# Performance work log

Measured on AMD Instinct MI355X. Metric: run time of the kernel, lower is better.

Reference implementation:

```python
import jax, jax.numpy as jnp
import numpy as np

B, S, D, H = 2, 2048, 1024, 16
Dh = D // H
EPS = 1e-6


def _layernorm(x, alpha, beta):
    # torch.std is unbiased (ddof=1); module divides by (std + eps)
    m = jnp.mean(x, axis=-1, keepdims=True)
    var = jnp.sum((x - m) ** 2, axis=-1, keepdims=True) / (x.shape[-1] - 1)
    return alpha * (x - m) / (jnp.sqrt(var) + EPS) + beta


def setup_inputs() -> dict:
    key = jax.random.key(0)
    ks = jax.random.split(key, 12)
    sc = 0.02
    return {
        "x": jax.random.normal(ks[0], (B, S, D), jnp.float32),
        "src_mask": jnp.ones((B, 1, S), jnp.int32),
        # per-head q/k/v projections stacked over heads: [H, D, Dh]
        "Wq": jax.random.normal(ks[1], (H, D, Dh), jnp.float32) * sc,
        "bq": jnp.zeros((H, Dh), jnp.float32),
        "Wk": jax.random.normal(ks[2], (H, D, Dh), jnp.float32) * sc,
        "bk": jnp.zeros((H, Dh), jnp.float32),
        "Wv": jax.random.normal(ks[3], (H, D, Dh), jnp.float32) * sc,
        "bv": jnp.zeros((H, Dh), jnp.float32),
        # FFN: D -> 4D -> D
        "W1": jax.random.normal(ks[4], (D, 4 * D), jnp.float32) * sc,
        "b1": jnp.zeros((4 * D,), jnp.float32),
        "W2": jax.random.normal(ks[5], (4 * D, D), jnp.float32) * sc,
        "b2": jnp.zeros((D,), jnp.float32),
        # two LayerNorms (residual connections)
        "alpha1": jnp.ones((D,), jnp.float32),
        "beta1": jnp.zeros((D,), jnp.float32),
        "alpha2": jnp.ones((D,), jnp.float32),
        "beta2": jnp.zeros((D,), jnp.float32),
    }


def _encoder_block(x, src_mask, Wq, bq, Wk, bk, Wv, bv, W1, b1, W2, b2,
                   alpha1, beta1, alpha2, beta2):
    # --- multi-head self-attention (all heads vectorized) ---
    q = jnp.einsum('bsd,hde->bhse', x, Wq) + bq[None, :, None, :]
    k = jnp.einsum('bsd,hde->bhse', x, Wk) + bk[None, :, None, :]
    v = jnp.einsum('bsd,hde->bhse', x, Wv) + bv[None, :, None, :]
    wei = jnp.einsum('bhse,bhte->bhst', q, k) * (Dh ** -0.5)  # [B,H,S,S]
    wei = jnp.where(src_mask[:, None, :, :] == 0, -jnp.inf, wei)
    wei = jax.nn.softmax(wei, axis=-1)
    attn = jnp.einsum('bhst,bhte->bhse', wei, v)  # [B,H,S,Dh]
    attn = attn.transpose(0, 2, 1, 3).reshape(x.shape[0], x.shape[1], D)
    # NOTE: original module never applies its output projection (self.pro unused)
    # residual 1: x + norm(sublayer(x))
    x = x + _layernorm(attn, alpha1, beta1)
    # --- feed-forward ---
    h = jax.nn.relu(x @ W1 + b1)
    ffn = h @ W2 + b2
    x = x + _layernorm(ffn, alpha2, beta2)
    return x


def reference(x, src_mask, Wq, bq, Wk, bk, Wv, bv, W1, b1, W2, b2,
              alpha1, beta1, alpha2, beta2):
    return _encoder_block(x, src_mask, Wq, bq, Wk, bk, Wv, bv,
                          W1, b1, W2, b2, alpha1, beta1, alpha2, beta2)
```

## Files before the change

kernel.cpp:

```cpp
#include <hip/hip_runtime.h>


#define DEV __device__ __forceinline__

typedef unsigned short u16;
typedef unsigned int u32;
typedef __attribute__((ext_vector_type(8))) short bfrag;
typedef __attribute__((ext_vector_type(8))) __bf16 bf16x8;
typedef __attribute__((ext_vector_type(2))) __bf16 bf16x2_t;
typedef __attribute__((ext_vector_type(4))) unsigned int u32x4;
typedef __attribute__((ext_vector_type(4))) float facc;
typedef __attribute__((ext_vector_type(16))) float facc16;

DEV float bf2f(u16 u) {
  unsigned int x = ((unsigned int)u) << 16;
  return __builtin_bit_cast(float, x);
}
DEV u16 f2bf(float f) {
  unsigned int x = __builtin_bit_cast(unsigned int, f);
  x += 0x7fffu + ((x >> 16) & 1u);
  return (u16)(x >> 16);
}

DEV void gl2lds16(const u16* g, u16* l) {
  auto gp = (const __attribute__((address_space(1))) unsigned int*)(g);
  auto lp = (__attribute__((address_space(3))) unsigned int*)(l);
  __builtin_amdgcn_global_load_lds(gp, lp, 16, 0, 0);
}

DEV facc mfma16(bfrag a, bfrag b, facc c) {
  return __builtin_amdgcn_mfma_f32_16x16x32_bf16(
      __builtin_bit_cast(bf16x8, a), __builtin_bit_cast(bf16x8, b), c, 0, 0, 0);
}

DEV facc16 mfma32(bfrag a, bfrag b, facc16 c) {
  return __builtin_amdgcn_mfma_f32_32x32x16_bf16(
      __builtin_bit_cast(bf16x8, a), __builtin_bit_cast(bf16x8, b), c, 0, 0, 0);
}

DEV u32 pk2(float a, float b) {
  bf16x2_t v;
  v[0] = (__bf16)a;
  v[1] = (__bf16)b;
  return __builtin_bit_cast(u32, v);
}

DEV void pswap(u32& a, u32& b) {
  asm volatile("v_permlane32_swap_b32 %0, %1" : "+v"(a), "+v"(b));
}

__global__ __launch_bounds__(256) void prep_kernel(
    const float* __restrict__ Wq, const float* __restrict__ Wk,
    const float* __restrict__ Wv, u16* __restrict__ WqkvT,
    const float* __restrict__ W1, u16* __restrict__ W1T,
    const float* __restrict__ W2, u16* __restrict__ W2T,
    const float* __restrict__ x, u16* __restrict__ xb) {
  __shared__ float tile[32][33];
  const int job = blockIdx.x;
  const int tr = threadIdx.x >> 5, tc = threadIdx.x & 31;

  if (job >= 11264) {
    const int i = (job - 11264) * 1024 + threadIdx.x * 4;
    const float4 v = *(const float4*)(x + i);
    ushort4 o;
    o.x = f2bf(v.x); o.y = f2bf(v.y); o.z = f2bf(v.z); o.w = f2bf(v.w);
    *(ushort4*)(xb + i) = o;
    return;
  }

  const float* in;
  u16* out;
  int C, R, c0, r0;
  if (job < 3072) {
    const int z = job >> 6, rem = job & 63;
    const int which = z >> 4, h = z & 15;
    in = ((which == 0) ? Wq : (which == 1) ? Wk : Wv) + (size_t)h * 1024 * 64;
    out = WqkvT + ((size_t)which * 1024 + h * 64) * 1024;
    C = 64; R = 1024;
    c0 = (rem & 1) * 32; r0 = (rem >> 1) * 32;
  } else if (job < 7168) {
    const int rem = job - 3072;
    in = W1; out = W1T; C = 4096; R = 1024;
    c0 = (rem & 127) * 32; r0 = (rem >> 7) * 32;
  } else {
    const int rem = job - 7168;
    in = W2; out = W2T; C = 1024; R = 4096;
    c0 = (rem & 31) * 32; r0 = (rem >> 5) * 32;
  }
#pragma unroll
  for (int k = 0; k < 4; k++)
    tile[tr + 8 * k][tc] = in[(size_t)(r0 + tr + 8 * k) * C + c0 + tc];
  __syncthreads();
#pragma unroll
  for (int k = 0; k < 4; k++)
    out[(size_t)(c0 + tr + 8 * k) * R + r0 + tc] = f2bf(tile[tc][tr + 8 * k]);
}

template <int MODE>
__global__ __launch_bounds__(512, 2) void gemm256(
    const u16* __restrict__ A, int lda, const u16* __restrict__ Bt, int ldb,
    int M, int N, int K,
    const float* __restrict__ bias0, const float* __restrict__ bias1,
    const float* __restrict__ bias2,
    void* __restrict__ out0, void* __restrict__ out1, void* __restrict__ out2) {
  __shared__ __align__(16) u16 As[2][256 * 64];
  __shared__ __align__(16) u16 Bs[2][256 * 64];
  const int tid = threadIdx.x;
  const int lane = tid & 63;
  const int wave = tid >> 6;
  const int laneM = lane & 15, quad = lane >> 4;
  const int kx = laneM & 7;
  const int m0 = blockIdx.x * 256, n0 = blockIdx.y * 256;
  const int wm = wave & 1, wn = wave >> 1;

  const u16* Ab = A;
  const u16* Bb = Bt;
  if (MODE == 3) {
    Ab += (size_t)blockIdx.z * K;
    Bb += (size_t)blockIdx.z * K;
  }

  int srow[4], skl[4];
#pragma unroll
  for (int c = 0; c < 4; c++) {
    const int slot = wave * 256 + c * 64 + lane;
    srow[c] = slot >> 3;
    skl[c] = ((slot & 7) ^ (srow[c] & 7)) * 8;
  }

  auto stage = [&](int X, int t) {
    const u16* Asrc = Ab + (size_t)t * 64;
    const u16* Bsrc = Bb + (size_t)t * 64;
#pragma unroll
    for (int c = 0; c < 4; c++)
      gl2lds16(Asrc + (size_t)(m0 + srow[c]) * lda + skl[c],
               As[X] + (size_t)(wave * 256 + c * 64) * 8);
#pragma unroll
    for (int c = 0; c < 4; c++)
      gl2lds16(Bsrc + (size_t)(n0 + srow[c]) * ldb + skl[c],
               Bs[X] + (size_t)(wave * 256 + c * 64) * 8);
  };

  facc acc[8][4] = {};

  const int NT = K >> 6;
  stage(0, 0);

  for (int t = 0; t < NT; ++t) {
    const int cur = t & 1;
    if (t + 1 < NT) {
      stage(cur ^ 1, t + 1);
      asm volatile("s_waitcnt vmcnt(8)" ::: "memory");
    } else {
      asm volatile("s_waitcnt vmcnt(0)" ::: "memory");
    }
    __builtin_amdgcn_s_barrier();

    const u16* as = As[cur];
    const u16* bs = Bs[cur];
#pragma unroll
    for (int k32 = 0; k32 < 2; ++k32) {
      bfrag af[8], bf[4];
#pragma unroll
      for (int i = 0; i < 8; i++) {
        const int row = wm * 128 + i * 16 + laneM;
        af[i] = *(const bfrag*)(as + row * 64 + (((k32 * 4 + quad) ^ kx) * 8));
      }
#pragma unroll
      for (int j = 0; j < 4; j++) {
        const int row = wn * 64 + j * 16 + laneM;
        bf[j] = *(const bfrag*)(bs + row * 64 + (((k32 * 4 + quad) ^ kx) * 8));
      }
#pragma unroll
      for (int i = 0; i < 8; i++)
#pragma unroll
        for (int j = 0; j < 4; j++)
          acc[i][j] = mfma16(af[i], bf[j], acc[i][j]);
    }
    __builtin_amdgcn_s_barrier();
  }

#pragma unroll
  for (int i = 0; i < 8; i++) {
#pragma unroll
    for (int j = 0; j < 4; j++) {
      const int col = n0 + wn * 64 + j * 16 + laneM;
      const int row0 = m0 + wm * 128 + i * 16 + quad * 4;
      if (MODE == 0) {
        const int which = col >> 10, c = col & 1023;
        const float* bp = (which == 0) ? bias0 : (which == 1) ? bias1 : bias2;
        u16* op = (u16*)((which == 0) ? out0 : (which == 1) ? out1 : out2);
        const float bb = bp[c];
        const int b = row0 >> 11, s0 = row0 & 2047;
        const int h = c >> 6, e = c & 63;
        if (which == 2) {
          ushort4 pk;
          pk.x = f2bf(acc[i][j][0] + bb);
          pk.y = f2bf(acc[i][j][1] + bb);
          pk.z = f2bf(acc[i][j][2] + bb);
          pk.w = f2bf(acc[i][j][3] + bb);
          *(ushort4*)(op + ((size_t)((b * 16 + h) * 64 + e)) * 2048 + s0) = pk;
        } else {
#pragma unroll
          for (int v = 0; v < 4; v++)
            op[((size_t)(b * 16 + h) * 2048 + s0 + v) * 64 + e] =
                f2bf(acc[i][j][v] + bb);
        }
      } else if (MODE == 1) {
        const float bb = bias0[col];
#pragma unroll
        for (int v = 0; v < 4; v++)
          ((u16*)out0)[(size_t)(row0 + v) * N + col] =
              f2bf(fmaxf(acc[i][j][v] + bb, 0.0f));
      } else {
        const int z = blockIdx.z;
        u16* op = (u16*)((z < 2) ? out0 : out1) + (size_t)(z & 1) * M * N;
#pragma unroll
        for (int v = 0; v < 4; v++)
          op[(size_t)(row0 + v) * N + col] = f2bf(acc[i][j][v]);
      }
    }
  }
}

__global__ __launch_bounds__(256) void attn_kernel(
    const u16* __restrict__ Qb, const u16* __restrict__ Kb,
    const u16* __restrict__ VTg, const int* __restrict__ mask,
    u16* __restrict__ Opart, float* __restrict__ lbuf) {
  __shared__ __align__(16) u16 KT[2][64 * 64];
  __shared__ __align__(16) u16 VS[2][64 * 64];
  __shared__ float MB[1024];
  const int tid = threadIdx.x;
  const int lane = tid & 63;
  const int wave = tid >> 6;
  const int col = lane & 31, hi = lane >> 5;
  const int bh = blockIdx.x, b = bh >> 4, h = bh & 15;
  const int q0 = blockIdx.y * 128;
  const int z = blockIdx.z;
  const int sbase = z * 1024;
  const u16* Qh = Qb + (size_t)bh * 2048 * 64;
  const u16* Kh = Kb + (size_t)bh * 2048 * 64 + (size_t)sbase * 64;
  const u16* Vh = VTg + (size_t)bh * 64 * 2048 + sbase;
  const float SC = 0.125f * 1.4426950408889634f;

  const int q = q0 + wave * 32 + col;
  bfrag qf[4];
#pragma unroll
  for (int ds = 0; ds < 4; ds++)
    qf[ds] = *(const bfrag*)(Qh + (size_t)q * 64 + ds * 16 + 8 * hi);

#pragma unroll
  for (int t = 0; t < 4; t++) {
    const int i = t * 256 + tid;
    MB[i] = mask[b * 2048 + sbase + i] ? 0.0f : -1e30f;
  }

  const int s0 = wave * 128;
  const int sl0 = s0 + lane, sl1 = s0 + 64 + lane;
  const int r0s = sl0 >> 3, c0s = ((sl0 & 7) ^ (r0s & 7)) * 8;
  const int r1s = sl1 >> 3, c1s = ((sl1 & 7) ^ (r1s & 7)) * 8;

  const int kx = col & 7;
  int off4[4];
#pragma unroll
  for (int i = 0; i < 4; i++) off4[i] = ((i * 2 + hi) ^ kx) << 3;

  gl2lds16(Kh + (size_t)r0s * 64 + c0s, KT[0] + (size_t)s0 * 8);
  gl2lds16(Kh + (size_t)r1s * 64 + c1s, KT[0] + (size_t)(s0 + 64) * 8);
  gl2lds16(Vh + (size_t)r0s * 2048 + c0s, VS[0] + (size_t)s0 * 8);
  gl2lds16(Vh + (size_t)r1s * 2048 + c1s, VS[0] + (size_t)(s0 + 64) * 8);
  __syncthreads();

  float lsum = 0.0f;
  facc16 oacc0 = (facc16)0.0f, oacc1 = (facc16)0.0f;

  for (int it = 0; it < 16; ++it) {
    const int t0 = it * 64;
    const int cur = it & 1;
    if (it < 15) {
      const int nxt = cur ^ 1;
      const int t0n = t0 + 64;
      gl2lds16(Kh + (size_t)(t0n + r0s) * 64 + c0s, KT[nxt] + (size_t)s0 * 8);
      gl2lds16(Kh + (size_t)(t0n + r1s) * 64 + c1s,
               KT[nxt] + (size_t)(s0 + 64) * 8);
      gl2lds16(Vh + (size_t)r0s * 2048 + t0n + c0s, VS[nxt] + (size_t)s0 * 8);
      gl2lds16(Vh + (size_t)r1s * 2048 + t0n + c1s,
               VS[nxt] + (size_t)(s0 + 64) * 8);
      asm volatile("s_waitcnt vmcnt(4)" ::: "memory");
    } else {
      asm volatile("s_waitcnt vmcnt(0)" ::: "memory");
    }
    __builtin_amdgcn_s_barrier();

    const u16* kb = KT[cur];
    const u16* vb = VS[cur];
#pragma unroll
    for (int tile = 0; tile < 2; tile++) {
      facc16 sacc = (facc16)0.0f;
#pragma unroll
      for (int ds = 0; ds < 4; ds++) {
        bfrag kf = *(const bfrag*)(kb + (tile * 32 + col) * 64 + off4[ds]);
        sacc = mfma32(kf, qf[ds], sacc);
      }
      u32 w[8];
#pragma unroll
      for (int g = 0; g < 4; g++) {
        const float4 mg = *(const float4*)(MB + t0 + tile * 32 + g * 8 + 4 * hi);
        const float p0 = __builtin_amdgcn_exp2f(fmaf(sacc[g * 4 + 0], SC, mg.x));
        const float p1 = __builtin_amdgcn_exp2f(fmaf(sacc[g * 4 + 1], SC, mg.y));
        const float p2 = __builtin_amdgcn_exp2f(fmaf(sacc[g * 4 + 2], SC, mg.z));
        const float p3 = __builtin_amdgcn_exp2f(fmaf(sacc[g * 4 + 3], SC, mg.w));
        lsum += (p0 + p1) + (p2 + p3);
        w[g * 2 + 0] = pk2(p0, p1);
        w[g * 2 + 1] = pk2(p2, p3);
      }
      pswap(w[0], w[2]);
      pswap(w[1], w[3]);
      pswap(w[4], w[6]);
      pswap(w[5], w[7]);
#pragma unroll
      for (int sub = 0; sub < 2; sub++) {
        u32x4 pv4;
        pv4[0] = w[sub * 4 + 0];
        pv4[1] = w[sub * 4 + 1];
        pv4[2] = w[sub * 4 + 2];
        pv4[3] = w[sub * 4 + 3];
        const bfrag pa = __builtin_bit_cast(bfrag, pv4);
        const int ks = tile * 2 + sub;
        {
          bfrag vf = *(const bfrag*)(vb + (0 * 32 + col) * 64 + off4[ks]);
          oacc0 = mfma32(vf, pa, oacc0);
        }
        {
          bfrag vf = *(const bfrag*)(vb + (1 * 32 + col) * 64 + off4[ks]);
          oacc1 = mfma32(vf, pa, oacc1);
        }
      }
    }
    __builtin_amdgcn_s_barrier();
  }

  const float l = lsum + __shfl_xor(lsum, 32, 64);
  if (hi == 0) lbuf[((size_t)(z * 32 + bh)) * 2048 + q] = l;

  u16* dst = Opart + (size_t)z * 4096 * 1024 +
             ((size_t)(b * 2048 + q)) * 1024 + h * 64;
#pragma unroll
  for (int eh = 0; eh < 2; eh++) {
    const facc16& oa = eh ? oacc1 : oacc0;
#pragma unroll
    for (int g = 0; g < 4; g++) {
      ushort4 pk;
      pk.x = f2bf(oa[g * 4 + 0]);
      pk.y = f2bf(oa[g * 4 + 1]);
      pk.z = f2bf(oa[g * 4 + 2]);
      pk.w = f2bf(oa[g * 4 + 3]);
      *(ushort4*)(dst + eh * 32 + g * 8 + 4 * hi) = pk;
    }
  }
}

__global__ __launch_bounds__(256) void ln_attn(
    const float* __restrict__ base, const u16* __restrict__ Opart,
    const float* __restrict__ lbuf,
    const float* __restrict__ alpha, const float* __restrict__ beta,
    float* __restrict__ outf, u16* __restrict__ outb) {
  __shared__ float red[4];
  const int row = blockIdx.x;
  const int t = threadIdx.x;
  const int b = row >> 11, s = row & 2047;
  const int h = t >> 4;
  const size_t off = (size_t)row * 1024 + t * 4;
  const size_t zstride = (size_t)4096 * 1024;

  const float l0 = lbuf[((size_t)(b * 16 + h)) * 2048 + s];
  const float l1 = lbuf[((size_t)(32 + b * 16 + h)) * 2048 + s];
  const float inv = 1.0f / (l0 + l1);

  const ushort4 o0 = *(const ushort4*)(Opart + off);
  const ushort4 o1 = *(const ushort4*)(Opart + zstride + off);
  float4 yv;
  yv.x = (bf2f(o0.x) + bf2f(o1.x)) * inv;
  yv.y = (bf2f(o0.y) + bf2f(o1.y)) * inv;
  yv.z = (bf2f(o0.z) + bf2f(o1.z)) * inv;
  yv.w = (bf2f(o0.w) + bf2f(o1.w)) * inv;

  float sm = yv.x + yv.y + yv.z + yv.w;
#pragma unroll
  for (int o = 1; o < 64; o <<= 1) sm += __shfl_xor(sm, o, 64);
  if ((t & 63) == 0) red[t >> 6] = sm;
  __syncthreads();
  const float mean = (red[0] + red[1] + red[2] + red[3]) * (1.0f / 1024.0f);
  __syncthreads();

  const float d0 = yv.x - mean, d1 = yv.y - mean, d2 = yv.z - mean, d3 = yv.w - mean;
  float ss = d0 * d0 + d1 * d1 + d2 * d2 + d3 * d3;
#pragma unroll
  for (int o = 1; o < 64; o <<= 1) ss += __shfl_xor(ss, o, 64);
  if ((t & 63) == 0) red[t >> 6] = ss;
  __syncthreads();
  const float var = (red[0] + red[1] + red[2] + red[3]) * (1.0f / 1023.0f);
  const float rstd = 1.0f / (sqrtf(var) + 1e-6f);

  const float4 bv = *(const float4*)(base + off);
  const float4 av = *(const float4*)(alpha + (size_t)t * 4);
  const float4 ev = *(const float4*)(beta + (size_t)t * 4);

  float4 ov;
  ov.x = bv.x + av.x * d0 * rstd + ev.x;
  ov.y = bv.y + av.y * d1 * rstd + ev.y;
  ov.z = bv.z + av.z * d2 * rstd + ev.z;
  ov.w = bv.w + av.w * d3 * rstd + ev.w;
  *(float4*)(outf + off) = ov;
  ushort4 ob;
  ob.x = f2bf(ov.x); ob.y = f2bf(ov.y); ob.z = f2bf(ov.z); ob.w = f2bf(ov.w);
  *(ushort4*)(outb + off) = ob;
}

__global__ __launch_bounds__(256) void ln_res2(
    const float* __restrict__ base, const u16* __restrict__ parts0,
    const u16* __restrict__ parts1, const float* __restrict__ biasv,
    const float* __restrict__ alpha, const float* __restrict__ beta,
    float* __restrict__ outf) {
  __shared__ float red[4];
  const int row = blockIdx.x;
  const int t = threadIdx.x;
  const size_t off = (size_t)row * 1024 + t * 4;
  const size_t stride = (size_t)4096 * 1024;

  float4 yv = *(const float4*)(biasv + (size_t)t * 4);
#pragma unroll
  for (int zi = 0; zi < 2; zi++) {
    const ushort4 pz = *(const ushort4*)(parts0 + zi * stride + off);
    yv.x += bf2f(pz.x); yv.y += bf2f(pz.y);
    yv.z += bf2f(pz.z); yv.w += bf2f(pz.w);
  }
#pragma unroll
  for (int zi = 0; zi < 2; zi++) {
    const ushort4 pz = *(const ushort4*)(parts1 + zi * stride + off);
    yv.x += bf2f(pz.x); yv.y += bf2f(pz.y);
    yv.z += bf2f(pz.z); yv.w += bf2f(pz.w);
  }

  float s = yv.x + yv.y + yv.z + yv.w;
#pragma unroll
  for (int o = 1; o < 64; o <<= 1) s += __shfl_xor(s, o, 64);
  if ((t & 63) == 0) red[t >> 6] = s;
  __syncthreads();
  const float mean = (red[0] + red[1] + red[2] + red[3]) * (1.0f / 1024.0f);
  __syncthreads();

  const float d0 = yv.x - mean, d1 = yv.y - mean, d2 = yv.z - mean, d3 = yv.w - mean;
  float ss = d0 * d0 + d1 * d1 + d2 * d2 + d3 * d3;
#pragma unroll
  for (int o = 1; o < 64; o <<= 1) ss += __shfl_xor(ss, o, 64);
  if ((t & 63) == 0) red[t >> 6] = ss;
  __syncthreads();
  const float var = (red[0] + red[1] + red[2] + red[3]) * (1.0f / 1023.0f);
  const float rstd = 1.0f / (sqrtf(var) + 1e-6f);

  const float4 bv = *(const float4*)(base + off);
  const float4 av = *(const float4*)(alpha + (size_t)t * 4);
  const float4 ev = *(const float4*)(beta + (size_t)t * 4);

  float4 ov;
  ov.x = bv.x + av.x * d0 * rstd + ev.x;
  ov.y = bv.y + av.y * d1 * rstd + ev.y;
  ov.z = bv.z + av.z * d2 * rstd + ev.z;
  ov.w = bv.w + av.w * d3 * rstd + ev.w;
  *(float4*)(outf + off) = ov;
}

extern "C" void kernel_launch(void* const* d_in, const int* in_sizes, int n_in,
                              void* d_out, int out_size, void* d_ws,
                              size_t ws_size, hipStream_t stream) {
  const float* x  = (const float*)d_in[0];
  const int* mask = (const int*)d_in[1];
  const float* Wq = (const float*)d_in[2];
  const float* bq = (const float*)d_in[3];
  const float* Wk = (const float*)d_in[4];
  const float* bk = (const float*)d_in[5];
  const float* Wv = (const float*)d_in[6];
  const float* bv = (const float*)d_in[7];
  const float* W1 = (const float*)d_in[8];
  const float* b1 = (const float*)d_in[9];
  const float* W2 = (const float*)d_in[10];
  const float* b2 = (const float*)d_in[11];
  const float* alpha1 = (const float*)d_in[12];
  const float* beta1  = (const float*)d_in[13];
  const float* alpha2 = (const float*)d_in[14];
  const float* beta2  = (const float*)d_in[15];
  float* out = (float*)d_out;

  char* p = (char*)d_ws;
  u16* xb      = (u16*)p;  p += (size_t)4096 * 1024 * 2;
  u16* WqkvT   = (u16*)p;  p += (size_t)3072 * 1024 * 2;
  u16* W1T     = (u16*)p;  p += (size_t)4096 * 1024 * 2;
  u16* W2T     = (u16*)p;  p += (size_t)1024 * 4096 * 2;
  u16* Qbuf    = (u16*)p;  p += (size_t)32 * 2048 * 64 * 2;
  u16* Kbuf    = (u16*)p;  p += (size_t)32 * 2048 * 64 * 2;
  u16* Vbuf    = (u16*)p;  p += (size_t)32 * 2048 * 64 * 2;
  u16* attnp   = (u16*)p;  p += (size_t)2 * 4096 * 1024 * 2;
  float* lbuf  = (float*)p; p += (size_t)2 * 32 * 2048 * 4;
  float* x1f   = (float*)p; p += (size_t)4096 * 1024 * 4;
  u16* x1b     = (u16*)p;  p += (size_t)4096 * 1024 * 2;
  u16* hbuf    = (u16*)p;  p += (size_t)4096 * 4096 * 2;
  u16* ffnp    = (u16*)p;  p += (size_t)2 * 4096 * 1024 * 2;

  prep_kernel<<<15360, 256, 0, stream>>>(Wq, Wk, Wv, WqkvT, W1, W1T, W2, W2T,
                                         x, xb);

  gemm256<0><<<dim3(16, 12), 512, 0, stream>>>(
      xb, 1024, WqkvT, 1024, 4096, 3072, 1024, bq, bk, bv, Qbuf, Kbuf, Vbuf);

  attn_kernel<<<dim3(32, 16, 2), 256, 0, stream>>>(Qbuf, Kbuf, Vbuf, mask,
                                                   attnp, lbuf);

  ln_attn<<<4096, 256, 0, stream>>>(x, attnp, lbuf, alpha1, beta1, x1f, x1b);

  gemm256<1><<<dim3(16, 16), 512, 0, stream>>>(
      x1b, 1024, W1T, 1024, 4096, 4096, 1024, b1, nullptr, nullptr,
      hbuf, nullptr, nullptr);

  gemm256<3><<<dim3(16, 4, 4), 512, 0, stream>>>(
      hbuf, 4096, W2T, 4096, 4096, 1024, 1024, nullptr, nullptr, nullptr,
      ffnp, attnp, nullptr);

  ln_res2<<<4096, 256, 0, stream>>>(x1f, ffnp, attnp, b2, alpha2, beta2, out);
}
```

Before: 312.8 us.

## Interleave GEMM prefetch with quarter-tile MFMA phases and raise wave priority

The GEMM main loop is split into four phases, each computing a quarter of the output tile (half of M by half of N). Each phase issues a quarter of the next K-tile's global-to-LDS loads, so memory traffic is spread across the compute instead of issued all at once. The staging layout is remapped so each phase loads whole row groups of A or B, and a barrier now follows every phase. s_setprio is raised around the MFMA bursts in both the GEMM and attention kernels to favour matrix-issuing waves. The risks are the extra barriers per K-step and the tighter vmcnt accounting.

Result: slower. 365.7 us (+16.9%).

```diff
diff --git a/kernel.cpp b/kernel.cpp
--- a/kernel.cpp
+++ b/kernel.cpp
@@ -120,64 +120,79 @@
     Bb += (size_t)blockIdx.z * K;
   }
 
-  int srow[4], skl[4];
-#pragma unroll
-  for (int c = 0; c < 4; c++) {
-    const int slot = wave * 256 + c * 64 + lane;
-    srow[c] = slot >> 3;
-    skl[c] = ((slot & 7) ^ (srow[c] & 7)) * 8;
-  }
-
-  auto stage = [&](int X, int t) {
-    const u16* Asrc = Ab + (size_t)t * 64;
-    const u16* Bsrc = Bb + (size_t)t * 64;
-#pragma unroll
-    for (int c = 0; c < 4; c++)
-      gl2lds16(Asrc + (size_t)(m0 + srow[c]) * lda + skl[c],
-               As[X] + (size_t)(wave * 256 + c * 64) * 8);
-#pragma unroll
-    for (int c = 0; c < 4; c++)
-      gl2lds16(Bsrc + (size_t)(n0 + srow[c]) * ldb + skl[c],
-               Bs[X] + (size_t)(wave * 256 + c * 64) * 8);
+  int srow[4], skl[4], sdst[4];
+#pragma unroll
+  for (int r = 0; r < 4; r++) {
+    const int slot = r * 512 + tid;
+    srow[r] = slot >> 3;
+    skl[r] = ((slot & 7) ^ (srow[r] & 7)) * 8;
+    sdst[r] = (r * 512 + wave * 64) * 8;
+  }
+
+  auto stagePhase = [&](int X, int t, int p) {
+    if (p < 2) {
+      const u16* Asrc = Ab + (size_t)t * 64;
+#pragma unroll
+      for (int rr = 2 * p; rr < 2 * p + 2; rr++)
+        gl2lds16(Asrc + (size_t)(m0 + srow[rr]) * lda + skl[rr],
+                 As[X] + sdst[rr]);
+    } else {
+      const u16* Bsrc = Bb + (size_t)t * 64;
+#pragma unroll
+      for (int rr = 2 * p - 4; rr < 2 * p - 2; rr++)
+        gl2lds16(Bsrc + (size_t)(n0 + srow[rr]) * ldb + skl[rr],
+                 Bs[X] + sdst[rr]);
+    }
   };
 
   facc acc[8][4] = {};
 
   const int NT = K >> 6;
-  stage(0, 0);
+#pragma unroll
+  for (int p = 0; p < 4; p++) stagePhase(0, 0, p);
 
   for (int t = 0; t < NT; ++t) {
-    const int cur = t & 1;
-    if (t + 1 < NT) {
-      stage(cur ^ 1, t + 1);
-      asm volatile("s_waitcnt vmcnt(8)" ::: "memory");
-    } else {
-      asm volatile("s_waitcnt vmcnt(0)" ::: "memory");
+    const int cur = t & 1, nxt = cur ^ 1;
+    const bool pf = (t + 1 < NT);
+
+#pragma unroll
+    for (int p = 0; p < 4; p++) {
+      if (pf) stagePhase(nxt, t + 1, p);
+      if (p == 0) {
+        if (pf) asm volatile("s_waitcnt vmcnt(2)" ::: "memory");
+        else    asm volatile("s_waitcnt vmcnt(0)" ::: "memory");
+        __builtin_amdgcn_s_barrier();
+      }
+      const int mh = p & 1, nh = p >> 1;
+      const u16* as = As[cur];
+      const u16* bs = Bs[cur];
+      bfrag af[2][4], bf[2][2];
+#pragma unroll
+      for (int k32 = 0; k32 < 2; k32++) {
+        const int ck = ((k32 * 4 + quad) ^ kx) * 8;
+#pragma unroll
+        for (int i = 0; i < 4; i++) {
+          const int row = wm * 128 + mh * 64 + i * 16 + laneM;
+          af[k32][i] = *(const bfrag*)(as + row * 64 + ck);
+        }
+#pragma unroll
+        for (int j = 0; j < 2; j++) {
+          const int row = wn * 64 + nh * 32 + j * 16 + laneM;
+          bf[k32][j] = *(const bfrag*)(bs + row * 64 + ck);
+        }
+      }
+      __builtin_amdgcn_s_setprio(1);
+#pragma unroll
+      for (int k32 = 0; k32 < 2; k32++)
+#pragma unroll
+        for (int i = 0; i < 4; i++)
+#pragma unroll
+          for (int j = 0; j < 2; j++)
+            acc[mh * 4 + i][nh * 2 + j] =
+                mfma16(af[k32][i], bf[k32][j], acc[mh * 4 + i][nh * 2 + j]);
+      __builtin_amdgcn_s_setprio(0);
+      __builtin_amdgcn_s_barrier();
     }
-    __builtin_amdgcn_s_barrier();
-
-    const u16* as = As[cur];
-    const u16* bs = Bs[cur];
-#pragma unroll
-    for (int k32 = 0; k32 < 2; ++k32) {
-      bfrag af[8], bf[4];
-#pragma unroll
-      for (int i = 0; i < 8; i++) {
-        const int row = wm * 128 + i * 16 + laneM;
-        af[i] = *(const bfrag*)(as + row * 64 + (((k32 * 4 + quad) ^ kx) * 8));
-      }
-#pragma unroll
-      for (int j = 0; j < 4; j++) {
-        const int row = wn * 64 + j * 16 + laneM;
-        bf[j] = *(const bfrag*)(bs + row * 64 + (((k32 * 4 + quad) ^ kx) * 8));
-      }
-#pragma unroll
-      for (int i = 0; i < 8; i++)
-#pragma unroll
-        for (int j = 0; j < 4; j++)
-          acc[i][j] = mfma16(af[i], bf[j], acc[i][j]);
-    }
-    __builtin_amdgcn_s_barrier();
   }
 
 #pragma unroll
@@ -297,11 +312,13 @@
 #pragma unroll
     for (int tile = 0; tile < 2; tile++) {
       facc16 sacc = (facc16)0.0f;
+      __builtin_amdgcn_s_setprio(1);
 #pragma unroll
       for (int ds = 0; ds < 4; ds++) {
         bfrag kf = *(const bfrag*)(kb + (tile * 32 + col) * 64 + off4[ds]);
         sacc = mfma32(kf, qf[ds], sacc);
       }
+      __builtin_amdgcn_s_setprio(0);
       u32 w[8];
 #pragma unroll
       for (int g = 0; g < 4; g++) {
@@ -318,6 +335,7 @@
       pswap(w[1], w[3]);
       pswap(w[4], w[6]);
       pswap(w[5], w[7]);
+      __builtin_amdgcn_s_setprio(1);
 #pragma unroll
       for (int sub = 0; sub < 2; sub++) {
         u32x4 pv4;
@@ -336,6 +354,7 @@
           oacc1 = mfma32(vf, pa, oacc1);
         }
       }
+      __builtin_amdgcn_s_setprio(0);
     }
     __builtin_amdgcn_s_barrier();
   }
```

## Interleave GEMM tile prefetch with MFMA quadrants and raise MFMA priority

Applied to the files above, without the earlier changes.

The GEMM main loop now splits each 64-wide K step into four quadrant sub-steps, each working on a 64x32 block of the wave's output. The next tile's global-to-LDS loads are issued in four slices, one between each pair of quadrants, instead of all at once before the compute. MFMA blocks are wrapped in s_setprio so that waves in their compute phase get issue priority. This is meant to spread memory traffic across the compute and cut stalls at each K step. In exchange it adds two extra barriers per iteration and a more complex register schedule for the A and B fragments.

After: 337.4 us. 1.08x slower.

```diff
diff --git a/kernel.cpp b/kernel.cpp
--- a/kernel.cpp
+++ b/kernel.cpp
@@ -128,55 +128,87 @@
     skl[c] = ((slot & 7) ^ (srow[c] & 7)) * 8;
   }
 
-  auto stage = [&](int X, int t) {
-    const u16* Asrc = Ab + (size_t)t * 64;
-    const u16* Bsrc = Bb + (size_t)t * 64;
-#pragma unroll
-    for (int c = 0; c < 4; c++)
-      gl2lds16(Asrc + (size_t)(m0 + srow[c]) * lda + skl[c],
-               As[X] + (size_t)(wave * 256 + c * 64) * 8);
-#pragma unroll
-    for (int c = 0; c < 4; c++)
-      gl2lds16(Bsrc + (size_t)(n0 + srow[c]) * ldb + skl[c],
-               Bs[X] + (size_t)(wave * 256 + c * 64) * 8);
+  auto stage2 = [&](int X, int t, int p) {
+#pragma unroll
+    for (int ci = 2 * p; ci < 2 * p + 2; ci++) {
+      if (ci < 4) {
+        gl2lds16(Ab + (size_t)t * 64 + (size_t)(m0 + srow[ci]) * lda + skl[ci],
+                 As[X] + (size_t)(wave * 256 + ci * 64) * 8);
+      } else {
+        const int c = ci - 4;
+        gl2lds16(Bb + (size_t)t * 64 + (size_t)(n0 + srow[c]) * ldb + skl[c],
+                 Bs[X] + (size_t)(wave * 256 + c * 64) * 8);
+      }
+    }
   };
 
   facc acc[8][4] = {};
+  bfrag af0[2][4], af1[2][4], bf0[2][2], bf1[2][2];
+
+  auto loadA = [&](bfrag (&af)[2][4], const u16* as, int mh) {
+#pragma unroll
+    for (int k32 = 0; k32 < 2; k32++) {
+      const int ck = ((k32 * 4 + quad) ^ kx) * 8;
+#pragma unroll
+      for (int i = 0; i < 4; i++)
+        af[k32][i] =
+            *(const bfrag*)(as + (wm * 128 + mh * 64 + i * 16 + laneM) * 64 + ck);
+    }
+  };
+  auto loadB = [&](bfrag (&bf)[2][2], const u16* bs, int nh) {
+#pragma unroll
+    for (int k32 = 0; k32 < 2; k32++) {
+      const int ck = ((k32 * 4 + quad) ^ kx) * 8;
+#pragma unroll
+      for (int j = 0; j < 2; j++)
+        bf[k32][j] =
+            *(const bfrag*)(bs + (wn * 64 + nh * 32 + j * 16 + laneM) * 64 + ck);
+    }
+  };
+  auto mmaQ = [&](bfrag (&af)[2][4], bfrag (&bf)[2][2], int mh, int nh) {
+    __builtin_amdgcn_s_setprio(1);
+#pragma unroll
+    for (int k32 = 0; k32 < 2; k32++)
+#pragma unroll
+      for (int i = 0; i < 4; i++)
+#pragma unroll
+        for (int j = 0; j < 2; j++)
+          acc[mh * 4 + i][nh * 2 + j] =
+              mfma16(af[k32][i], bf[k32][j], acc[mh * 4 + i][nh * 2 + j]);
+    __builtin_amdgcn_s_setprio(0);
+  };
 
   const int NT = K >> 6;
-  stage(0, 0);
+#pragma unroll
+  for (int p = 0; p < 4; p++) stage2(0, 0, p);
 
   for (int t = 0; t < NT; ++t) {
-    const int cur = t & 1;
-    if (t + 1 < NT) {
-      stage(cur ^ 1, t + 1);
-      asm volatile("s_waitcnt vmcnt(8)" ::: "memory");
+    const int cur = t & 1, nxt = cur ^ 1;
+    const bool pf = (t + 1 < NT);
+    const u16* as = As[cur];
+    const u16* bs = Bs[cur];
+
+    if (pf) {
+      stage2(nxt, t + 1, 0);
+      asm volatile("s_waitcnt vmcnt(2)" ::: "memory");
     } else {
       asm volatile("s_waitcnt vmcnt(0)" ::: "memory");
     }
     __builtin_amdgcn_s_barrier();
-
-    const u16* as = As[cur];
-    const u16* bs = Bs[cur];
-#pragma unroll
-    for (int k32 = 0; k32 < 2; ++k32) {
-      bfrag af[8], bf[4];
-#pragma unroll
-      for (int i = 0; i < 8; i++) {
-        const int row = wm * 128 + i * 16 + laneM;
-        af[i] = *(const bfrag*)(as + row * 64 + (((k32 * 4 + quad) ^ kx) * 8));
-      }
-#pragma unroll
-      for (int j = 0; j < 4; j++) {
-        const int row = wn * 64 + j * 16 + laneM;
-        bf[j] = *(const bfrag*)(bs + row * 64 + (((k32 * 4 + quad) ^ kx) * 8));
-      }
-#pragma unroll
-      for (int i = 0; i < 8; i++)
-#pragma unroll
-        for (int j = 0; j < 4; j++)
-          acc[i][j] = mfma16(af[i], bf[j], acc[i][j]);
-    }
+    loadA(af0, as, 0);
+    loadB(bf0, bs, 0);
+    mmaQ(af0, bf0, 0, 0);
+    __builtin_amdgcn_s_barrier();
+    if (pf) stage2(nxt, t + 1, 1);
+    loadA(af1, as, 1);
+    mmaQ(af1, bf0, 1, 0);
+    __builtin_amdgcn_s_barrier();
+    if (pf) stage2(nxt, t + 1, 2);
+    loadB(bf1, bs, 1);
+    mmaQ(af1, bf1, 1, 1);
+    __builtin_amdgcn_s_barrier();
+    if (pf) stage2(nxt, t + 1, 3);
+    mmaQ(af0, bf1, 0, 1);
     __builtin_amdgcn_s_barrier();
   }
 
```

## Shrink GEMM tiles to 128x128 and halve split-K for the FFN down-projection

Applied to the files above, without the earlier changes.

Replaces the 256x256-tile GEMM with a 128x128-tile variant: 512 threads per block, half the LDS, and occupancy raised to 4 blocks. The smaller tiles give many more blocks per GEMM, which should fill all CUs on the MI355X instead of the 192 or 256 blocks launched before. The W2 GEMM drops from 4-way to 2-way split-K, so the final layernorm reads only two bf16 partial buffers. In exchange, each block reuses less data per tile, adding global and LDS traffic per FLOP, and each wave has fewer MFMAs to hide latency behind.

After: 316.0 us. Within noise of the previous version (+1.0%).

```diff
diff --git a/kernel.cpp b/kernel.cpp
--- a/kernel.cpp
+++ b/kernel.cpp
@@ -97,20 +97,20 @@
 }
 
 template <int MODE>
-__global__ __launch_bounds__(512, 2) void gemm256(
+__global__ __launch_bounds__(512, 4) void gemm128(
     const u16* __restrict__ A, int lda, const u16* __restrict__ Bt, int ldb,
     int M, int N, int K,
     const float* __restrict__ bias0, const float* __restrict__ bias1,
     const float* __restrict__ bias2,
     void* __restrict__ out0, void* __restrict__ out1, void* __restrict__ out2) {
-  __shared__ __align__(16) u16 As[2][256 * 64];
-  __shared__ __align__(16) u16 Bs[2][256 * 64];
+  __shared__ __align__(16) u16 As[2][128 * 64];
+  __shared__ __align__(16) u16 Bs[2][128 * 64];
   const int tid = threadIdx.x;
   const int lane = tid & 63;
   const int wave = tid >> 6;
   const int laneM = lane & 15, quad = lane >> 4;
   const int kx = laneM & 7;
-  const int m0 = blockIdx.x * 256, n0 = blockIdx.y * 256;
+  const int m0 = blockIdx.x * 128, n0 = blockIdx.y * 128;
   const int wm = wave & 1, wn = wave >> 1;
 
   const u16* Ab = A;
@@ -120,28 +120,28 @@
     Bb += (size_t)blockIdx.z * K;
   }
 
-  int srow[4], skl[4];
-#pragma unroll
-  for (int c = 0; c < 4; c++) {
-    const int slot = wave * 256 + c * 64 + lane;
-    srow[c] = slot >> 3;
-    skl[c] = ((slot & 7) ^ (srow[c] & 7)) * 8;
+  int srow[2], skl[2];
+#pragma unroll
+  for (int r = 0; r < 2; r++) {
+    const int slot = r * 512 + tid;
+    srow[r] = slot >> 3;
+    skl[r] = ((slot & 7) ^ (srow[r] & 7)) * 8;
   }
 
   auto stage = [&](int X, int t) {
     const u16* Asrc = Ab + (size_t)t * 64;
     const u16* Bsrc = Bb + (size_t)t * 64;
 #pragma unroll
-    for (int c = 0; c < 4; c++)
-      gl2lds16(Asrc + (size_t)(m0 + srow[c]) * lda + skl[c],
-               As[X] + (size_t)(wave * 256 + c * 64) * 8);
-#pragma unroll
-    for (int c = 0; c < 4; c++)
-      gl2lds16(Bsrc + (size_t)(n0 + srow[c]) * ldb + skl[c],
-               Bs[X] + (size_t)(wave * 256 + c * 64) * 8);
+    for (int r = 0; r < 2; r++)
+      gl2lds16(Asrc + (size_t)(m0 + srow[r]) * lda + skl[r],
+               As[X] + (size_t)(r * 512 + wave * 64) * 8);
+#pragma unroll
+    for (int r = 0; r < 2; r++)
+      gl2lds16(Bsrc + (size_t)(n0 + srow[r]) * ldb + skl[r],
+               Bs[X] + (size_t)(r * 512 + wave * 64) * 8);
   };
 
-  facc acc[8][4] = {};
+  facc acc[4][2] = {};
 
   const int NT = K >> 6;
   stage(0, 0);
@@ -150,7 +150,7 @@
     const int cur = t & 1;
     if (t + 1 < NT) {
       stage(cur ^ 1, t + 1);
-      asm volatile("s_waitcnt vmcnt(8)" ::: "memory");
+      asm volatile("s_waitcnt vmcnt(4)" ::: "memory");
     } else {
       asm volatile("s_waitcnt vmcnt(0)" ::: "memory");
     }
@@ -160,32 +160,33 @@
     const u16* bs = Bs[cur];
 #pragma unroll
     for (int k32 = 0; k32 < 2; ++k32) {
-      bfrag af[8], bf[4];
-#pragma unroll
-      for (int i = 0; i < 8; i++) {
-        const int row = wm * 128 + i * 16 + laneM;
-        af[i] = *(const bfrag*)(as + row * 64 + (((k32 * 4 + quad) ^ kx) * 8));
+      const int ck = ((k32 * 4 + quad) ^ kx) * 8;
+      bfrag af[4], bf[2];
+#pragma unroll
+      for (int i = 0; i < 4; i++) {
+        const int row = wm * 64 + i * 16 + laneM;
+        af[i] = *(const bfrag*)(as + row * 64 + ck);
       }
 #pragma unroll
-      for (int j = 0; j < 4; j++) {
-        const int row = wn * 64 + j * 16 + laneM;
-        bf[j] = *(const bfrag*)(bs + row * 64 + (((k32 * 4 + quad) ^ kx) * 8));
+      for (int j = 0; j < 2; j++) {
+        const int row = wn * 32 + j * 16 + laneM;
+        bf[j] = *(const bfrag*)(bs + row * 64 + ck);
       }
 #pragma unroll
-      for (int i = 0; i < 8; i++)
-#pragma unroll
-        for (int j = 0; j < 4; j++)
+      for (int i = 0; i < 4; i++)
+#pragma unroll
+        for (int j = 0; j < 2; j++)
           acc[i][j] = mfma16(af[i], bf[j], acc[i][j]);
     }
     __builtin_amdgcn_s_barrier();
   }
 
 #pragma unroll
-  for (int i = 0; i < 8; i++) {
-#pragma unroll
-    for (int j = 0; j < 4; j++) {
-      const int col = n0 + wn * 64 + j * 16 + laneM;
-      const int row0 = m0 + wm * 128 + i * 16 + quad * 4;
+  for (int i = 0; i < 4; i++) {
+#pragma unroll
+    for (int j = 0; j < 2; j++) {
+      const int col = n0 + wn * 32 + j * 16 + laneM;
+      const int row0 = m0 + wm * 64 + i * 16 + quad * 4;
       if (MODE == 0) {
         const int which = col >> 10, c = col & 1023;
         const float* bp = (which == 0) ? bias0 : (which == 1) ? bias1 : bias2;
@@ -213,8 +214,7 @@
           ((u16*)out0)[(size_t)(row0 + v) * N + col] =
               f2bf(fmaxf(acc[i][j][v] + bb, 0.0f));
       } else {
-        const int z = blockIdx.z;
-        u16* op = (u16*)((z < 2) ? out0 : out1) + (size_t)(z & 1) * M * N;
+        u16* op = (u16*)out0 + (size_t)blockIdx.z * M * N;
 #pragma unroll
         for (int v = 0; v < 4; v++)
           op[(size_t)(row0 + v) * N + col] = f2bf(acc[i][j][v]);
@@ -418,8 +418,8 @@
 }
 
 __global__ __launch_bounds__(256) void ln_res2(
-    const float* __restrict__ base, const u16* __restrict__ parts0,
-    const u16* __restrict__ parts1, const float* __restrict__ biasv,
+    const float* __restrict__ base, const u16* __restrict__ parts,
+    const float* __restrict__ biasv,
     const float* __restrict__ alpha, const float* __restrict__ beta,
     float* __restrict__ outf) {
   __shared__ float red[4];
@@ -431,13 +431,7 @@
   float4 yv = *(const float4*)(biasv + (size_t)t * 4);
 #pragma unroll
   for (int zi = 0; zi < 2; zi++) {
-    const ushort4 pz = *(const ushort4*)(parts0 + zi * stride + off);
-    yv.x += bf2f(pz.x); yv.y += bf2f(pz.y);
-    yv.z += bf2f(pz.z); yv.w += bf2f(pz.w);
-  }
-#pragma unroll
-  for (int zi = 0; zi < 2; zi++) {
-    const ushort4 pz = *(const ushort4*)(parts1 + zi * stride + off);
+    const ushort4 pz = *(const ushort4*)(parts + zi * stride + off);
     yv.x += bf2f(pz.x); yv.y += bf2f(pz.y);
     yv.z += bf2f(pz.z); yv.w += bf2f(pz.w);
   }
@@ -510,7 +504,7 @@
   prep_kernel<<<15360, 256, 0, stream>>>(Wq, Wk, Wv, WqkvT, W1, W1T, W2, W2T,
                                          x, xb);
 
-  gemm256<0><<<dim3(16, 12), 512, 0, stream>>>(
+  gemm128<0><<<dim3(32, 24), 512, 0, stream>>>(
       xb, 1024, WqkvT, 1024, 4096, 3072, 1024, bq, bk, bv, Qbuf, Kbuf, Vbuf);
 
   attn_kernel<<<dim3(32, 16, 2), 256, 0, stream>>>(Qbuf, Kbuf, Vbuf, mask,
@@ -518,13 +512,13 @@
 
   ln_attn<<<4096, 256, 0, stream>>>(x, attnp, lbuf, alpha1, beta1, x1f, x1b);
 
-  gemm256<1><<<dim3(16, 16), 512, 0, stream>>>(
+  gemm128<1><<<dim3(32, 32), 512, 0, stream>>>(
       x1b, 1024, W1T, 1024, 4096, 4096, 1024, b1, nullptr, nullptr,
       hbuf, nullptr, nullptr);
 
-  gemm256<3><<<dim3(16, 4, 4), 512, 0, stream>>>(
-      hbuf, 4096, W2T, 4096, 4096, 1024, 1024, nullptr, nullptr, nullptr,
-      ffnp, attnp, nullptr);
-
-  ln_res2<<<4096, 256, 0, stream>>>(x1f, ffnp, attnp, b2, alpha2, beta2, out);
-}
+  gemm128<3><<<dim3(32, 8, 2), 512, 0, stream>>>(
+      hbuf, 4096, W2T, 4096, 4096, 1024, 2048, nullptr, nullptr, nullptr,
+      ffnp, nullptr, nullptr);
+
+  ln_res2<<<4096, 256, 0, stream>>>(x1f, ffnp, b2, alpha2, beta2, out);
+}
```
